# Performance work log

Measured on AMD Instinct MI355X. Metric: run time of the kernel, lower is better.

Reference implementation:

```python
import jax, jax.numpy as jnp
import numpy as np

# Chambolle-Pock / Condat over-relaxed primal-dual constants (from _TVDenoiser.__init__)
TAU = 0.01
RHO = 1.99
SIGMA = 1.0 / TAU / 8.0  # 1/tau/8, 8 = Lipschitz const of D^T D in 2D
THS = 0.1                # lambda (denoise threshold)
NITER = 40
CRIT = 1e-5


def nabla2(x):
    """Forward finite differences: x (..., H, W) -> u (..., H, W, 2).
    Channel 0: diff along H (rows), channel 1: diff along W (cols); last
    row/col of each channel is zero (as in the deepinv original)."""
    dh = jnp.zeros_like(x).at[..., :-1, :].set(x[..., 1:, :] - x[..., :-1, :])
    dw = jnp.zeros_like(x).at[..., :, :-1].set(x[..., :, 1:] - x[..., :, :-1])
    return jnp.stack([dh, dw], axis=-1)


def nabla2_adjoint(u):
    """Adjoint of nabla2: u (..., H, W, 2) -> (..., H, W)."""
    v0 = u[..., :-1, :, 0]  # (..., H-1, W)
    v1 = u[..., :, :-1, 1]  # (..., H, W-1)
    out = jnp.zeros(u.shape[:-1], u.dtype)
    out = out.at[..., :-1, :].add(-v0).at[..., 1:, :].add(v0)
    out = out.at[..., :, :-1].add(-v1).at[..., :, 1:].add(v1)
    return out


def _step(x2, u2, y):
    # prox_tau_fx: (x + tau*y)/(1+tau)
    x = (x2 - TAU * nabla2_adjoint(u2) + TAU * y) / (1.0 + TAU)
    # prox_sigma_g_conj: project gradient field onto L2 ball of radius lambda
    v = u2 + SIGMA * nabla2(2.0 * x - x2)
    mag = jnp.sqrt(jnp.sum(v * v, axis=-1))  # (..., H, W)
    u = v / jnp.maximum(mag / THS, 1.0)[..., None]
    # over-relaxation
    x2n = x2 + RHO * (x - x2)
    u2n = u2 + RHO * (u - u2)
    return x2n, u2n


def setup_inputs() -> dict:
    key = jax.random.key(0)
    y = jax.random.normal(key, (8, 512, 512), dtype=jnp.float32)
    return {"y": y}


def reference(y):
    # warm restart init: x2 = y, u2 = 0 (restart branch of forward)
    u0 = jnp.zeros(y.shape + (2,), y.dtype)

    def cond(state):
        x2, u2, it, rel = state
        # original breaks at end of iteration _ if _ > 1 and rel_err < crit
        return (it < NITER) & jnp.logical_not((it >= 3) & (rel < CRIT))

    def body(state):
        x2, u2, it, _ = state
        x2n, u2n = _step(x2, u2, y)
        rel = jnp.linalg.norm((x2 - x2n).ravel()) / jnp.linalg.norm(
            x2n.ravel() + 1e-12
        )
        return (x2n, u2n, it + 1, rel)

    x2, u2, it, rel = jax.lax.while_loop(
        cond, body, (y, u0, jnp.int32(0), jnp.float32(jnp.inf))
    )
    return x2
```

## Files before the change

kernel.cpp:

```cpp
#include <hip/hip_runtime.h>


#define Hh 512
#define Ww 512
#define Bb 8
#define TS 48
#define KF 8
#define S  64
#define NT 512
#define RS 8

__global__ __launch_bounds__(NT, 3)
void tv_fused(const float*  __restrict__ x2_in,
              const float2* __restrict__ u_in,
              const float*  __restrict__ y_in,
              float*  __restrict__ x2_out,
              float2* __restrict__ u_out,
              int first, int last)
{
    constexpr float TAU = 0.01f;
    constexpr float RHO = 1.99f;
    constexpr float HRHO = 0.995f;
    constexpr float SIGMA = 12.5f;
    constexpr float THS = 0.1f;
    constexpr float INV_1PT = 1.0f / 1.01f;

    __shared__ float u0B [9 * S];
    __shared__ float wTop[9 * S];

    const int b   = blockIdx.z;
    const int r0  = blockIdx.y * TS;
    const int c0  = blockIdx.x * TS;
    const int tid = threadIdx.x;
    const size_t plane = (size_t)b * (Hh * Ww);

    const int s   = tid >> 6;
    const int lc  = tid & 63;
    const int gc  = c0 - KF + lc;
    const bool colin = (gc >= 0) & (gc < Ww);
    const float sewf = (gc < Ww - 1) ? SIGMA : 0.f;
    const int lr0 = RS * s;
    const int gr0 = r0 - KF + lr0;
    const float sigBot = (gr0 + RS - 1 == Hh - 1) ? 0.f : SIGMA;

    if (tid < S) { u0B[tid] = 0.f; wTop[8 * S + tid] = 0.f; }

    float u0[RS], u1[RS], x2[RS], yv[RS], w[RS];
    unsigned tmp0 = 0u, tmp1 = 0u;

    #pragma unroll
    for (int i = 0; i < RS; ++i) {
        const int gr = gr0 + i;
        const int lr = lr0 + i;
        const bool img = colin & (gr >= 0) & (gr < Hh);
        float a = 0.f, c = 0.f, z0 = 0.f, z1 = 0.f;
        if (img) {
            size_t gi = plane + (size_t)gr * Ww + gc;
            c = y_in[gi];
            if (first) a = c;
            else {
                a = x2_in[gi];
                float2 uu = u_in[gi];
                z0 = uu.x; z1 = uu.y;
            }
        }
        u0[i] = z0; u1[i] = z1; x2[i] = a; yv[i] = c;
        unsigned tm = img ? (unsigned)min(min(lr, S - 1 - lr), min(lc, S - 1 - lc)) : 0u;
        if (i < 4) tmp0 |= tm << (8 * i);
        else       tmp1 |= tm << (8 * (i - 4));
    }
    u0B[(s + 1) * S + lc] = u0[RS - 1];
    __syncthreads();

    for (int t = 0; t < KF; ++t) {
        {
            float u0a = u0B[s * S + lc];
            #pragma unroll
            for (int i = 0; i < RS; ++i) {
                float ul = __shfl_up(u1[i], 1, 64);
                float ua = (i == 0) ? u0a : u0[i - 1];
                float adj = ua - u0[i] + ul - u1[i];
                float xv = fmaf(TAU, yv[i] - adj, x2[i]);
                w[i] = fmaf(2.0f * INV_1PT, xv, -x2[i]);
            }
            wTop[s * S + lc] = w[0];
        }
        __syncthreads();
        {
            float wbot = wTop[(s + 1) * S + lc];
            #pragma unroll
            for (int i = 0; i < RS; ++i) {
                float wr = __shfl_down(w[i], 1, 64);
                float wb = (i == RS - 1) ? wbot : w[i + 1];
                const float sig_h = (i == RS - 1) ? sigBot : SIGMA;
                float v0 = fmaf(sig_h, wb - w[i], u0[i]);
                float v1 = fmaf(sewf,  wr - w[i], u1[i]);
                float iv = fminf(THS * __builtin_amdgcn_rsqf(fmaf(v0, v0, v1 * v1)), 1.f);
                unsigned tmb = ((i < 4 ? tmp0 : tmp1) >> (8 * (i & 3))) & 255u;
                bool act = (unsigned)t < tmb;
                float r1 = act ? RHO  : 0.f;
                float rh = act ? HRHO : 0.f;
                u0[i] = fmaf(r1, fmaf(v0, iv, -u0[i]), u0[i]);
                u1[i] = fmaf(r1, fmaf(v1, iv, -u1[i]), u1[i]);
                x2[i] = fmaf(rh, w[i] - x2[i], x2[i]);
            }
            u0B[(s + 1) * S + lc] = u0[RS - 1];
        }
        __syncthreads();
    }

    if (s >= 1 && s <= 6 && lc >= KF && lc < KF + TS && gc < Ww) {
        #pragma unroll
        for (int i = 0; i < RS; ++i) {
            const int gr = gr0 + i;
            if (gr < Hh) {
                size_t gi = plane + (size_t)gr * Ww + gc;
                x2_out[gi] = x2[i];
                if (!last) u_out[gi] = make_float2(u0[i], u1[i]);
            }
        }
    }
}

extern "C" void kernel_launch(void* const* d_in, const int* in_sizes, int n_in,
                              void* d_out, int out_size, void* d_ws, size_t ws_size,
                              hipStream_t stream)
{
    const float* y = (const float*)d_in[0];
    float* out = (float*)d_out;
    const size_t NP = (size_t)Bb * Hh * Ww;

    float*  ws  = (float*)d_ws;
    float*  x2A = ws;
    float*  x2B = ws + NP;
    float2* uA  = (float2*)(ws + 2 * NP);
    float2* uB  = (float2*)(ws + 4 * NP);

    dim3 grid((Ww + TS - 1) / TS, (Hh + TS - 1) / TS, Bb);

    tv_fused<<<grid, NT, 0, stream>>>(y,   uB, y, x2A, uA, 1, 0);
    tv_fused<<<grid, NT, 0, stream>>>(x2A, uA, y, x2B, uB, 0, 0);
    tv_fused<<<grid, NT, 0, stream>>>(x2B, uB, y, x2A, uA, 0, 0);
    tv_fused<<<grid, NT, 0, stream>>>(x2A, uA, y, x2B, uB, 0, 0);
    tv_fused<<<grid, NT, 0, stream>>>(x2B, uB, y, out, uA, 0, 1);
}
```

Measured before the change: 231.5 us.

## Halve per-iteration barriers by recomputing halo w from exchanged neighbour state

Each warp-row strip now receives the neighbour strip's first-row x2/u0/u1 through double-buffered shared memory and recomputes the halo w value locally, instead of exchanging w in a separate phase. This drops one __syncthreads per inner iteration (two down to one) and removes the barrier on the last iteration. In exchange it adds redundant arithmetic for the halo row, an extra y load per thread, and more shared-memory traffic and footprint.

```diff
diff --git a/kernel.cpp b/kernel.cpp
--- a/kernel.cpp
+++ b/kernel.cpp
@@ -25,8 +25,10 @@
     constexpr float THS = 0.1f;
     constexpr float INV_1PT = 1.0f / 1.01f;
 
-    __shared__ float u0B [9 * S];
-    __shared__ float wTop[9 * S];
+    __shared__ float uaB[2][8 * S];
+    __shared__ float hx2[2][8 * S];
+    __shared__ float hu0[2][8 * S];
+    __shared__ float hu1[2][8 * S];
 
     const int b   = blockIdx.z;
     const int r0  = blockIdx.y * TS;
@@ -43,7 +45,12 @@
     const int gr0 = r0 - KF + lr0;
     const float sigBot = (gr0 + RS - 1 == Hh - 1) ? 0.f : SIGMA;
 
-    if (tid < S) { u0B[tid] = 0.f; wTop[8 * S + tid] = 0.f; }
+    if (tid < S) {
+        uaB[0][tid] = 0.f;           uaB[1][tid] = 0.f;
+        hx2[0][7 * S + tid] = 0.f;   hx2[1][7 * S + tid] = 0.f;
+        hu0[0][7 * S + tid] = 0.f;   hu0[1][7 * S + tid] = 0.f;
+        hu1[0][7 * S + tid] = 0.f;   hu1[1][7 * S + tid] = 0.f;
+    }
 
     float u0[RS], u1[RS], x2[RS], yv[RS], w[RS];
     unsigned tmp0 = 0u, tmp1 = 0u;
@@ -69,44 +76,70 @@
         if (i < 4) tmp0 |= tm << (8 * i);
         else       tmp1 |= tm << (8 * (i - 4));
     }
-    u0B[(s + 1) * S + lc] = u0[RS - 1];
+    float yvh = 0.f;
+    {
+        const int gr = gr0 + RS;
+        if ((s < 7) & colin & (gr < Hh)) yvh = y_in[plane + (size_t)gr * Ww + gc];
+    }
+
+    if (s < 7) uaB[0][(s + 1) * S + lc] = u0[RS - 1];
+    if (s > 0) {
+        hx2[0][(s - 1) * S + lc] = x2[0];
+        hu0[0][(s - 1) * S + lc] = u0[0];
+        hu1[0][(s - 1) * S + lc] = u1[0];
+    }
     __syncthreads();
 
     for (int t = 0; t < KF; ++t) {
+        const int rb = t & 1;
+        const int wbuf = rb ^ 1;
+        float ua0 = uaB[rb][s * S + lc];
+        float x2h = hx2[rb][s * S + lc];
+        float u0h = hu0[rb][s * S + lc];
+        float u1h = hu1[rb][s * S + lc];
+
+        #pragma unroll
+        for (int i = 0; i < RS; ++i) {
+            float ul = __shfl_up(u1[i], 1, 64);
+            float ua = (i == 0) ? ua0 : u0[i - 1];
+            float adj = ua - u0[i] + ul - u1[i];
+            float xv = fmaf(TAU, yv[i] - adj, x2[i]);
+            w[i] = fmaf(2.0f * INV_1PT, xv, -x2[i]);
+        }
+        float wh;
         {
-            float u0a = u0B[s * S + lc];
-            #pragma unroll
-            for (int i = 0; i < RS; ++i) {
-                float ul = __shfl_up(u1[i], 1, 64);
-                float ua = (i == 0) ? u0a : u0[i - 1];
-                float adj = ua - u0[i] + ul - u1[i];
-                float xv = fmaf(TAU, yv[i] - adj, x2[i]);
-                w[i] = fmaf(2.0f * INV_1PT, xv, -x2[i]);
+            float ul = __shfl_up(u1h, 1, 64);
+            float adj = u0[RS - 1] - u0h + ul - u1h;
+            float xv = fmaf(TAU, yvh - adj, x2h);
+            wh = fmaf(2.0f * INV_1PT, xv, -x2h);
+        }
+
+        #pragma unroll
+        for (int i = 0; i < RS; ++i) {
+            float wr = __shfl_down(w[i], 1, 64);
+            float wbv = (i == RS - 1) ? wh : w[i + 1];
+            const float sig_h = (i == RS - 1) ? sigBot : SIGMA;
+            float v0 = fmaf(sig_h, wbv - w[i], u0[i]);
+            float v1 = fmaf(sewf,  wr - w[i], u1[i]);
+            float iv = fminf(THS * __builtin_amdgcn_rsqf(fmaf(v0, v0, v1 * v1)), 1.f);
+            unsigned tmb = ((i < 4 ? tmp0 : tmp1) >> (8 * (i & 3))) & 255u;
+            bool act = (unsigned)t < tmb;
+            float r1 = act ? RHO  : 0.f;
+            float rh = act ? HRHO : 0.f;
+            u0[i] = fmaf(r1, fmaf(v0, iv, -u0[i]), u0[i]);
+            u1[i] = fmaf(r1, fmaf(v1, iv, -u1[i]), u1[i]);
+            x2[i] = fmaf(rh, w[i] - x2[i], x2[i]);
+        }
+
+        if (t < KF - 1) {
+            if (s < 7) uaB[wbuf][(s + 1) * S + lc] = u0[RS - 1];
+            if (s > 0) {
+                hx2[wbuf][(s - 1) * S + lc] = x2[0];
+                hu0[wbuf][(s - 1) * S + lc] = u0[0];
+                hu1[wbuf][(s - 1) * S + lc] = u1[0];
             }
-            wTop[s * S + lc] = w[0];
+            __syncthreads();
         }
-        __syncthreads();
-        {
-            float wbot = wTop[(s + 1) * S + lc];
-            #pragma unroll
-            for (int i = 0; i < RS; ++i) {
-                float wr = __shfl_down(w[i], 1, 64);
-                float wb = (i == RS - 1) ? wbot : w[i + 1];
-                const float sig_h = (i == RS - 1) ? sigBot : SIGMA;
-                float v0 = fmaf(sig_h, wb - w[i], u0[i]);
-                float v1 = fmaf(sewf,  wr - w[i], u1[i]);
-                float iv = fminf(THS * __builtin_amdgcn_rsqf(fmaf(v0, v0, v1 * v1)), 1.f);
-                unsigned tmb = ((i < 4 ? tmp0 : tmp1) >> (8 * (i & 3))) & 255u;
-                bool act = (unsigned)t < tmb;
-                float r1 = act ? RHO  : 0.f;
-                float rh = act ? HRHO : 0.f;
-                u0[i] = fmaf(r1, fmaf(v0, iv, -u0[i]), u0[i]);
-                u1[i] = fmaf(r1, fmaf(v1, iv, -u1[i]), u1[i]);
-                x2[i] = fmaf(rh, w[i] - x2[i], x2[i]);
-            }
-            u0B[(s + 1) * S + lc] = u0[RS - 1];
-        }
-        __syncthreads();
     }
 
     if (s >= 1 && s <= 6 && lc >= KF && lc < KF + TS && gc < Ww) {
```

Result: slower. 247.4 us (+6.8%).
